# Optimization experiments

Measured on AMD Instinct MI355X. Metric: run time of the kernel, lower is better.

The kernel has to match this reference:

```python
import jax, jax.numpy as jnp
import numpy as np
import math

EMB, HID, SEQ, BATCH, VOCAB, LAYERS = 512, 1024, 128, 64, 10000, 2


def setup_inputs() -> dict:
    key = jax.random.key(0)
    ks = jax.random.split(key, 8)
    bnd = math.sqrt(1.0 / HID)
    return {
        "inputs": jax.random.randint(ks[0], (SEQ, BATCH), 0, VOCAB),
        "hidden": jnp.zeros((LAYERS, BATCH, HID), jnp.float32),
        "emb": jax.random.uniform(ks[1], (VOCAB, EMB), jnp.float32, -0.1, 0.1),
        "W_x0": jax.random.uniform(ks[2], (EMB, HID), jnp.float32, -bnd, bnd),
        "W_x1": jax.random.uniform(ks[3], (HID, HID), jnp.float32, -bnd, bnd),
        "W_h": jax.random.uniform(ks[4], (LAYERS, HID, HID), jnp.float32, -bnd, bnd),
        "b_h": jax.random.uniform(ks[5], (LAYERS, HID), jnp.float32, -bnd, bnd),
        "W_out": jax.random.uniform(ks[6], (HID, VOCAB), jnp.float32, -0.1, 0.1),
        "b_out": jnp.zeros((VOCAB,), jnp.float32),
    }


def reference(inputs, hidden, emb, W_x0, W_x1, W_h, b_h, W_out, b_out):
    # Stacked vanilla RNN over time; dropout is identity (dp_keep_prob=1.0).
    scale = jnp.asarray(math.sqrt(EMB), jnp.float32)  # WordEmbedding * sqrt(n_units)

    def step(h, tok):
        # h: (L, B, H); tok: (B,)
        x = emb[tok] * scale                                   # (B, E)
        h0 = jnp.tanh(x @ W_x0 + h[0] @ W_h[0] + b_h[0])       # (B, H)
        h1 = jnp.tanh(h0 @ W_x1 + h[1] @ W_h[1] + b_h[1])      # (B, H)
        logits_t = h1 @ W_out + b_out                          # (B, V)
        return jnp.stack([h0, h1]), logits_t

    final_hidden, logits = jax.lax.scan(step, hidden, inputs)
    return logits, final_hidden
```

## Files before the change

kernel.cpp:

```cpp
#include <hip/hip_runtime.h>
#include <math.h>


typedef unsigned short u16;
typedef unsigned long long u64;
typedef __bf16 bf16x8 __attribute__((ext_vector_type(8)));
typedef float  f32x4  __attribute__((ext_vector_type(4)));
typedef unsigned int u32x4 __attribute__((ext_vector_type(4)));
typedef u16 u16x8 __attribute__((ext_vector_type(8)));

#define SEQ_ 128
#define B_   64
#define E_   512
#define H_   1024
#define V_   10000
#define VP_  10112
#define ROWS_ (SEQ_*B_)
#define BH_  (B_*H_)
#define LOGITS_ 81920000
#define NWG_ 192
#define FPS_ (129*32)

__device__ __forceinline__ u16 f2bf(float f) {
  unsigned u = __builtin_bit_cast(unsigned, f);
  u += 0x7fffu + ((u >> 16) & 1u);
  return (u16)(u >> 16);
}
__device__ __forceinline__ float bf2f(u16 h) {
  unsigned u = ((unsigned)h) << 16;
  return __builtin_bit_cast(float, u);
}
__device__ __forceinline__ void st64(void* p, u64 v) {
  __hip_atomic_store((u64*)p, v, __ATOMIC_RELAXED, __HIP_MEMORY_SCOPE_AGENT);
}
__device__ __forceinline__ u64 pk64(float a, float b) {
  return (u64)__builtin_bit_cast(unsigned, a) |
         ((u64)__builtin_bit_cast(unsigned, b) << 32);
}
__device__ __forceinline__ float tanh_fast(float x) {
  float e = __expf(2.0f * x);
  return 1.0f - 2.0f * __builtin_amdgcn_rcpf(e + 1.0f);
}


__global__ __launch_bounds__(256)
void transpose_split(const float* __restrict__ in, u16* __restrict__ outHi,
                     u16* __restrict__ outLo, int K, int N, int NP)
{
  __shared__ float tile[32][33];
  const int n0 = blockIdx.x * 32, k0 = blockIdx.y * 32;
  const int x = threadIdx.x & 31;
  const int y = threadIdx.x >> 5;
  (void)NP;
#pragma unroll
  for (int i = 0; i < 4; ++i) {
    const int r = y * 4 + i;
    const int n = n0 + x;
    tile[r][x] = (n < N) ? in[(size_t)(k0 + r) * N + n] : 0.f;
  }
  __syncthreads();
#pragma unroll
  for (int i = 0; i < 4; ++i) {
    const int r = y * 4 + i;
    const int n = n0 + r;
    const int k = k0 + x;
    const float v = tile[x][r];
    const u16 hb = f2bf(v);
    outHi[(size_t)n * K + k] = hb;
    if (outLo) outLo[(size_t)n * K + k] = f2bf(v - bf2f(hb));
  }
}

__global__ __launch_bounds__(256)
void gather_x(const int* __restrict__ toks, const float* __restrict__ emb,
              u16* __restrict__ XBhi, u16* __restrict__ XBlo)
{
  const int tid = blockIdx.x * 256 + threadIdx.x;
  const int row = tid >> 6;
  const int c8 = (tid & 63) * 8;
  const int tok = toks[row];
  const float* e = emb + (size_t)tok * E_ + c8;
  u16x8 hv, lv;
#pragma unroll
  for (int j = 0; j < 8; ++j) {
    float f = e[j] * 22.627416997969522f;
    u16 hb = f2bf(f);
    hv[j] = hb;
    lv[j] = f2bf(f - bf2f(hb));
  }
  *(u16x8*)(XBhi + (size_t)row * E_ + c8) = hv;
  *(u16x8*)(XBlo + (size_t)row * E_ + c8) = lv;
}

__global__ __launch_bounds__(256)
void hid_cast(const float* __restrict__ h, u16* H0hi, u16* H0lo, u16* H1hi, u16* H1lo)
{
  const int tid = blockIdx.x * 256 + threadIdx.x;
  float v0 = h[tid], v1 = h[BH_ + tid];
  u16 a = f2bf(v0); H0hi[tid] = a; H0lo[tid] = f2bf(v0 - bf2f(a));
  u16 b = f2bf(v1); H1hi[tid] = b; H1lo[tid] = f2bf(v1 - bf2f(b));
}

template<int NPASS>
__global__ __launch_bounds__(256)
void gemm_bf16(const u16* __restrict__ Ahi, const u16* __restrict__ Alo,
               const u16* __restrict__ Bhi, const u16* __restrict__ Blo,
               const float* __restrict__ bias, float* __restrict__ C,
               int K, int Nreal, int ldc, int nbx, int nby)
{
  constexpr int LDT = 40;
  __shared__ u16 lds[(NPASS == 3 ? 4 : 2) * 128 * LDT];
  u16* As  = lds;
  u16* Bs  = lds + 128 * LDT;
  u16* As2 = (NPASS == 3) ? (lds + 2 * 128 * LDT) : lds;
  u16* Bs2 = (NPASS == 3) ? (lds + 3 * 128 * LDT) : lds;

  const int S = 8;
  int bid  = blockIdx.x;
  int scol = bid / (S * nby);
  int rem  = bid - scol * (S * nby);
  int w    = nbx - scol * S; if (w > S) w = S;
  int bx   = scol * S + rem % w;
  int by   = rem / w;
  const int m0 = by * 128, n0 = bx * 128;

  const int tid  = threadIdx.x;
  const int wave = tid >> 6, lane = tid & 63;
  const int wm = (wave & 1) * 64, wn = (wave >> 1) * 64;
  const int lrow = lane & 15, lk = (lane >> 4) * 8;

  f32x4 acc[4][4] = {};

  const int kTiles = K >> 5;
  for (int kt = 0; kt < kTiles; ++kt) {
    const int k0 = kt << 5;
    __syncthreads();
#pragma unroll
    for (int c = tid; c < 512; c += 256) {
      const int row = c >> 2, kq = c & 3;
      const int l = row * LDT + kq * 8;
      *(u32x4*)(As + l) = *(const u32x4*)(Ahi + (size_t)(m0 + row) * K + k0 + kq * 8);
      *(u32x4*)(Bs + l) = *(const u32x4*)(Bhi + (size_t)(n0 + row) * K + k0 + kq * 8);
      if constexpr (NPASS == 3) {
        *(u32x4*)(As2 + l) = *(const u32x4*)(Alo + (size_t)(m0 + row) * K + k0 + kq * 8);
        *(u32x4*)(Bs2 + l) = *(const u32x4*)(Blo + (size_t)(n0 + row) * K + k0 + kq * 8);
      }
    }
    __syncthreads();
    bf16x8 a[4], b[4];
#pragma unroll
    for (int i = 0; i < 4; ++i) {
      a[i] = *(const bf16x8*)(As + (wm + i * 16 + lrow) * LDT + lk);
      b[i] = *(const bf16x8*)(Bs + (wn + i * 16 + lrow) * LDT + lk);
    }
    if constexpr (NPASS == 3) {
      bf16x8 a2[4], b2[4];
#pragma unroll
      for (int i = 0; i < 4; ++i) {
        a2[i] = *(const bf16x8*)(As2 + (wm + i * 16 + lrow) * LDT + lk);
        b2[i] = *(const bf16x8*)(Bs2 + (wn + i * 16 + lrow) * LDT + lk);
      }
#pragma unroll
      for (int mi = 0; mi < 4; ++mi)
#pragma unroll
        for (int ni = 0; ni < 4; ++ni) {
          acc[mi][ni] = __builtin_amdgcn_mfma_f32_16x16x32_bf16(a[mi],  b[ni],  acc[mi][ni], 0, 0, 0);
          acc[mi][ni] = __builtin_amdgcn_mfma_f32_16x16x32_bf16(a[mi],  b2[ni], acc[mi][ni], 0, 0, 0);
          acc[mi][ni] = __builtin_amdgcn_mfma_f32_16x16x32_bf16(a2[mi], b[ni],  acc[mi][ni], 0, 0, 0);
        }
    } else {
#pragma unroll
      for (int mi = 0; mi < 4; ++mi)
#pragma unroll
        for (int ni = 0; ni < 4; ++ni)
          acc[mi][ni] = __builtin_amdgcn_mfma_f32_16x16x32_bf16(a[mi], b[ni], acc[mi][ni], 0, 0, 0);
    }
  }
#pragma unroll
  for (int mi = 0; mi < 4; ++mi)
#pragma unroll
    for (int ni = 0; ni < 4; ++ni)
#pragma unroll
      for (int r = 0; r < 4; ++r) {
        const int row = m0 + wm + mi * 16 + (lane >> 4) * 4 + r;
        const int col = n0 + wn + ni * 16 + lrow;
        if (col < Nreal) {
          float v = acc[mi][ni][r];
          if (bias) v += bias[col];
          C[(size_t)row * ldc + col] = v;
        }
      }
}

__device__ __forceinline__ void publishWG(unsigned* f, int wgi)
{
  asm volatile("s_waitcnt vmcnt(0)" ::: "memory");
  __syncthreads();
  if (threadIdx.x == 0)
    __hip_atomic_store(f + wgi, 1u, __ATOMIC_RELAXED, __HIP_MEMORY_SCOPE_AGENT);
}
__device__ __forceinline__ void pollG(const unsigned* f)
{
  if (threadIdx.x < 64) {
    int it = 0;
    for (;;) {
      unsigned v = __hip_atomic_load(f + (threadIdx.x & 31),
                                     __ATOMIC_RELAXED, __HIP_MEMORY_SCOPE_AGENT);
      if (__all(v != 0)) break;
      if (it < 4) __builtin_amdgcn_s_sleep(2);
      else        __builtin_amdgcn_s_sleep(8);
      ++it;
    }
  }
  __syncthreads();
}
__device__ __forceinline__ void pollG2(const unsigned* fA, const unsigned* fB)
{
  if (threadIdx.x < 64) {
    int it = 0;
    bool okA = false, okB = false;
    for (;;) {
      const int l = threadIdx.x & 31;
      if (!okA) okA = __all(__hip_atomic_load(fA + l, __ATOMIC_RELAXED,
                                              __HIP_MEMORY_SCOPE_AGENT) != 0);
      if (!okB) okB = __all(__hip_atomic_load(fB + l, __ATOMIC_RELAXED,
                                              __HIP_MEMORY_SCOPE_AGENT) != 0);
      if (okA && okB) break;
      if (it < 4) __builtin_amdgcn_s_sleep(2);
      else        __builtin_amdgcn_s_sleep(8);
      ++it;
    }
  }
  __syncthreads();
}

__device__ __forceinline__ f32x4 gemm96(const u16* __restrict__ Ahi,
                                        const u16* __restrict__ Alo,
                                        const u16* bsp, int xorv, int lk8,
                                        size_t aoff, f32x4 acc0)
{
  f32x4 acc1 = {0.f, 0.f, 0.f, 0.f};
  f32x4 acc2 = {0.f, 0.f, 0.f, 0.f};
#pragma unroll
  for (int kc = 0; kc < 32; ++kc) {
    bf16x8 ah = *(const bf16x8*)(Ahi + aoff + kc * 32);
    bf16x8 al = *(const bf16x8*)(Alo + aoff + kc * 32);
    bf16x8 bh = *(const bf16x8*)(bsp + ((kc * 32 + lk8) ^ xorv));
    bf16x8 bl = *(const bf16x8*)(bsp + 32768 + ((kc * 32 + lk8) ^ xorv));
    acc0 = __builtin_amdgcn_mfma_f32_16x16x32_bf16(bh, ah, acc0, 0, 0, 0);
    acc1 = __builtin_amdgcn_mfma_f32_16x16x32_bf16(bl, ah, acc1, 0, 0, 0);
    acc2 = __builtin_amdgcn_mfma_f32_16x16x32_bf16(bh, al, acc2, 0, 0, 0);
  }
  return acc0 + acc1 + acc2;
}

__global__ __launch_bounds__(256, 1)
void recur_roles(const u16* __restrict__ Wh0h, const u16* __restrict__ Wh0l,
                 const u16* __restrict__ Wx1h, const u16* __restrict__ Wx1l,
                 const u16* __restrict__ Wh1h, const u16* __restrict__ Wh1l,
                 const float* __restrict__ XP0, const float* __restrict__ b1,
                 float* __restrict__ Pbuf,
                 u16* __restrict__ H0hi, u16* __restrict__ H0lo,
                 u16* __restrict__ H1hi, u16* __restrict__ H1lo,
                 float* __restrict__ final0, float* __restrict__ final1,
                 unsigned* __restrict__ flags)
{
  __shared__ u16 bsm[2 * 32 * 1024];

  const int wg   = blockIdx.x;
  const int role = wg >> 6;
  const int idx  = wg & 63;
  const int bg   = idx >> 5, cg = idx & 31;

  const u16* Bhi = (role == 0) ? Wh0h : (role == 1) ? Wx1h : Wh1h;
  const u16* Blo = (role == 0) ? Wh0l : (role == 1) ? Wx1l : Wh1l;

  const int tid  = threadIdx.x;
  const int wv   = tid >> 6, lane = tid & 63;
  const int wbg  = wv >> 1, wcg = wv & 1;
  const int lb   = lane & 15;
  const int lk8  = (lane >> 4) * 8;

  for (int c = tid; c < 8192; c += 256) {
    const int p   = c >> 12;
    const int cc  = c & 4095;
    const int col = cc >> 7;
    const int k8  = (cc & 127) * 8;
    u32x4 v = *(const u32x4*)((p ? Blo : Bhi) + (size_t)(cg * 32 + col) * H_ + k8);
    *(u32x4*)(bsm + p * 32768 + col * 1024 + (k8 ^ ((col & 7) << 3))) = v;
  }
  __syncthreads();

  const int batch = bg * 32 + wbg * 16 + lb;
  const int c0    = cg * 32 + wcg * 16 + (lk8 >> 1);
  const int colL  = wcg * 16 + lb;
  const int xorv  = (colL & 7) << 3;
  const u16* bsp  = bsm + colL * 1024;
  const size_t aoff = (size_t)batch * H_ + lk8;
  const size_t boff = (size_t)batch * H_ + c0;

  unsigned* flg0 = flags;
  unsigned* flgP = flags + 2 * FPS_;
  unsigned* flg1 = flags + 4 * FPS_;

  if (role == 0) {
    for (int t = 0; t < SEQ_; ++t) {
      f32x4 init = *(const f32x4*)(XP0 + (size_t)t * BH_ + boff);
      if (t >= 1) pollG(flg0 + ((size_t)bg * 129 + t) * 32);
      f32x4 acc = gemm96(H0hi + (size_t)t * BH_, H0lo + (size_t)t * BH_,
                         bsp, xorv, lk8, aoff, init);
      u64 whi = 0, wlo = 0; float hv[4];
#pragma unroll
      for (int r = 0; r < 4; ++r) {
        float v = tanh_fast(acc[r]);
        u16 hb = f2bf(v);
        whi |= (u64)hb << (16 * r);
        wlo |= (u64)f2bf(v - bf2f(hb)) << (16 * r);
        hv[r] = v;
      }
      st64(H0hi + (size_t)(t + 1) * BH_ + boff, whi);
      st64(H0lo + (size_t)(t + 1) * BH_ + boff, wlo);
      if (t == SEQ_ - 1) {
        st64(final0 + boff,     pk64(hv[0], hv[1]));
        st64(final0 + boff + 2, pk64(hv[2], hv[3]));
      }
      publishWG(flg0 + ((size_t)bg * 129 + (t + 1)) * 32, cg);
    }
  } else if (role == 1) {
    const f32x4 binit = *(const f32x4*)(b1 + c0);
    for (int s = 1; s <= SEQ_; ++s) {
      pollG(flg0 + ((size_t)bg * 129 + s) * 32);
      f32x4 acc = gemm96(H0hi + (size_t)s * BH_, H0lo + (size_t)s * BH_,
                         bsp, xorv, lk8, aoff, binit);
      float* op = Pbuf + (size_t)(s - 1) * BH_ + boff;
      st64(op,     pk64(acc[0], acc[1]));
      st64(op + 2, pk64(acc[2], acc[3]));
      publishWG(flgP + ((size_t)bg * 129 + s) * 32, cg);
    }
  } else {
    for (int s = 1; s <= SEQ_; ++s) {
      if (s >= 2) pollG2(flgP + ((size_t)bg * 129 + s) * 32,
                         flg1 + ((size_t)bg * 129 + (s - 1)) * 32);
      else        pollG (flgP + ((size_t)bg * 129 + s) * 32);
      f32x4 init = *(const f32x4*)(Pbuf + (size_t)(s - 1) * BH_ + boff);
      f32x4 acc = gemm96(H1hi + (size_t)(s - 1) * BH_, H1lo + (size_t)(s - 1) * BH_,
                         bsp, xorv, lk8, aoff, init);
      u64 whi = 0, wlo = 0; float hv[4];
#pragma unroll
      for (int r = 0; r < 4; ++r) {
        float v = tanh_fast(acc[r]);
        u16 hb = f2bf(v);
        whi |= (u64)hb << (16 * r);
        wlo |= (u64)f2bf(v - bf2f(hb)) << (16 * r);
        hv[r] = v;
      }
      st64(H1hi + (size_t)s * BH_ + boff, whi);
      st64(H1lo + (size_t)s * BH_ + boff, wlo);
      if (s == SEQ_) {
        st64(final1 + boff,     pk64(hv[0], hv[1]));
        st64(final1 + boff + 2, pk64(hv[2], hv[3]));
      }
      publishWG(flg1 + ((size_t)bg * 129 + s) * 32, cg);
    }
  }
}

extern "C" void kernel_launch(void* const* d_in, const int* in_sizes, int n_in,
                              void* d_out, int out_size, void* d_ws, size_t ws_size,
                              hipStream_t stream)
{
  (void)in_sizes; (void)n_in; (void)out_size; (void)ws_size;
  const int*   toks = (const int*)d_in[0];
  const float* hid0 = (const float*)d_in[1];
  const float* emb  = (const float*)d_in[2];
  const float* Wx0  = (const float*)d_in[3];
  const float* Wx1  = (const float*)d_in[4];
  const float* Wh   = (const float*)d_in[5];
  const float* bh   = (const float*)d_in[6];
  const float* Wout = (const float*)d_in[7];
  const float* bout = (const float*)d_in[8];
  float* out = (float*)d_out;

  char* ws = (char*)d_ws;
  size_t off = 0;
  auto alloc = [&](size_t bytes) -> void* {
    void* p = ws + off;
    off += (bytes + 255) & ~(size_t)255;
    return p;
  };
  unsigned* flags = (unsigned*)alloc(6 * FPS_ * 4);
  u16* XBhi  = (u16*)alloc((size_t)ROWS_ * E_ * 2);
  u16* XBlo  = (u16*)alloc((size_t)ROWS_ * E_ * 2);
  u16* Wx0Th = (u16*)alloc((size_t)H_ * E_ * 2);
  u16* Wx0Tl = (u16*)alloc((size_t)H_ * E_ * 2);
  u16* Wx1Th = (u16*)alloc((size_t)H_ * H_ * 2);
  u16* Wx1Tl = (u16*)alloc((size_t)H_ * H_ * 2);
  u16* Wh0Th = (u16*)alloc((size_t)H_ * H_ * 2);
  u16* Wh0Tl = (u16*)alloc((size_t)H_ * H_ * 2);
  u16* Wh1Th = (u16*)alloc((size_t)H_ * H_ * 2);
  u16* Wh1Tl = (u16*)alloc((size_t)H_ * H_ * 2);
  u16* WoutT = (u16*)alloc((size_t)VP_ * H_ * 2);
  float* XP0 = (float*)alloc((size_t)ROWS_ * H_ * 4);
  float* Pbuf= (float*)alloc((size_t)SEQ_ * BH_ * 4);
  u16* H0hi  = (u16*)alloc((size_t)(SEQ_ + 1) * BH_ * 2);
  u16* H0lo  = (u16*)alloc((size_t)(SEQ_ + 1) * BH_ * 2);
  u16* H1hi  = (u16*)alloc((size_t)(SEQ_ + 1) * BH_ * 2);
  u16* H1lo  = (u16*)alloc((size_t)(SEQ_ + 1) * BH_ * 2);

  hipMemsetAsync(flags, 0, 6 * FPS_ * 4, stream);
  transpose_split<<<dim3(H_ / 32, E_ / 32), 256, 0, stream>>>(Wx0, Wx0Th, Wx0Tl, E_, H_, H_);
  transpose_split<<<dim3(H_ / 32, H_ / 32), 256, 0, stream>>>(Wx1, Wx1Th, Wx1Tl, H_, H_, H_);
  transpose_split<<<dim3(H_ / 32, H_ / 32), 256, 0, stream>>>(Wh,           Wh0Th, Wh0Tl, H_, H_, H_);
  transpose_split<<<dim3(H_ / 32, H_ / 32), 256, 0, stream>>>(Wh + H_ * H_, Wh1Th, Wh1Tl, H_, H_, H_);
  transpose_split<<<dim3(VP_ / 32, H_ / 32), 256, 0, stream>>>(Wout, WoutT, nullptr, H_, V_, VP_);
  gather_x<<<ROWS_ * E_ / 8 / 256, 256, 0, stream>>>(toks, emb, XBhi, XBlo);
  hid_cast<<<BH_ / 256, 256, 0, stream>>>(hid0, H0hi, H0lo, H1hi, H1lo);

  gemm_bf16<3><<<8 * 64, 256, 0, stream>>>(XBhi, XBlo, Wx0Th, Wx0Tl, bh, XP0,
                                           E_, H_, H_, 8, 64);
  recur_roles<<<NWG_, 256, 0, stream>>>(Wh0Th, Wh0Tl, Wx1Th, Wx1Tl, Wh1Th, Wh1Tl,
                                        XP0, bh + H_, Pbuf,
                                        H0hi, H0lo, H1hi, H1lo,
                                        out + LOGITS_, out + LOGITS_ + BH_, flags);
  gemm_bf16<1><<<79 * 64, 256, 0, stream>>>(H1hi + BH_, nullptr, WoutT, nullptr,
                                            bout, out, H_, V_, V_, 79, 64);
}
```

Before: 2.027 ms.

## Map recurrence role groups to XCDs and poll same-XCD flags via L2

Launches 256 workgroups and uses the round-robin block-to-XCD assignment so each (role, batch-group) of 32 workgroups sits on one XCD, with two XCDs' worth of blocks exiting immediately. Flags produced and consumed within the same XCD are polled with sc0 loads that hit the shared L2, with a periodic agent-scope load as a fallback; cross-XCD waits keep agent-scope polling with shorter sleeps. The intent is lower step-to-step handoff latency in the serial recurrence. It relies on the undocumented dispatch order of blocks to XCDs and on L2 coherence for correctness and speed, and the H data written by other workgroups is still read through normal loads.

```diff
diff --git a/kernel.cpp b/kernel.cpp
--- a/kernel.cpp
+++ b/kernel.cpp
@@ -18,7 +18,6 @@
 #define ROWS_ (SEQ_*B_)
 #define BH_  (B_*H_)
 #define LOGITS_ 81920000
-#define NWG_ 192
 #define FPS_ (129*32)
 
 __device__ __forceinline__ u16 f2bf(float f) {
@@ -40,6 +39,13 @@
 __device__ __forceinline__ float tanh_fast(float x) {
   float e = __expf(2.0f * x);
   return 1.0f - 2.0f * __builtin_amdgcn_rcpf(e + 1.0f);
+}
+__device__ __forceinline__ unsigned ld_sc0(const unsigned* p) {
+  unsigned v;
+  asm volatile("global_load_dword %0, %1, off sc0\n\t"
+               "s_waitcnt vmcnt(0)"
+               : "=v"(v) : "v"(p) : "memory");
+  return v;
 }
 
 
@@ -199,35 +205,33 @@
   if (threadIdx.x == 0)
     __hip_atomic_store(f + wgi, 1u, __ATOMIC_RELAXED, __HIP_MEMORY_SCOPE_AGENT);
 }
-__device__ __forceinline__ void pollG(const unsigned* f)
+__device__ __forceinline__ void pollL(const unsigned* f)
 {
   if (threadIdx.x < 64) {
+    const int l = threadIdx.x & 31;
+    for (int it = 0;; ++it) {
+      unsigned v;
+      if ((it & 15) == 15)
+        v = __hip_atomic_load(f + l, __ATOMIC_RELAXED, __HIP_MEMORY_SCOPE_AGENT);
+      else
+        v = ld_sc0(f + l);
+      if (__all(v != 0)) break;
+      __builtin_amdgcn_s_sleep(1);
+    }
+  }
+  __syncthreads();
+}
+__device__ __forceinline__ void pollR(const unsigned* f)
+{
+  if (threadIdx.x < 64) {
+    const int l = threadIdx.x & 31;
     int it = 0;
     for (;;) {
-      unsigned v = __hip_atomic_load(f + (threadIdx.x & 31),
-                                     __ATOMIC_RELAXED, __HIP_MEMORY_SCOPE_AGENT);
+      unsigned v = __hip_atomic_load(f + l, __ATOMIC_RELAXED,
+                                     __HIP_MEMORY_SCOPE_AGENT);
       if (__all(v != 0)) break;
-      if (it < 4) __builtin_amdgcn_s_sleep(2);
-      else        __builtin_amdgcn_s_sleep(8);
-      ++it;
-    }
-  }
-  __syncthreads();
-}
-__device__ __forceinline__ void pollG2(const unsigned* fA, const unsigned* fB)
-{
-  if (threadIdx.x < 64) {
-    int it = 0;
-    bool okA = false, okB = false;
-    for (;;) {
-      const int l = threadIdx.x & 31;
-      if (!okA) okA = __all(__hip_atomic_load(fA + l, __ATOMIC_RELAXED,
-                                              __HIP_MEMORY_SCOPE_AGENT) != 0);
-      if (!okB) okB = __all(__hip_atomic_load(fB + l, __ATOMIC_RELAXED,
-                                              __HIP_MEMORY_SCOPE_AGENT) != 0);
-      if (okA && okB) break;
-      if (it < 4) __builtin_amdgcn_s_sleep(2);
-      else        __builtin_amdgcn_s_sleep(8);
+      if (it < 4) __builtin_amdgcn_s_sleep(1);
+      else        __builtin_amdgcn_s_sleep(4);
       ++it;
     }
   }
@@ -267,10 +271,12 @@
 {
   __shared__ u16 bsm[2 * 32 * 1024];
 
-  const int wg   = blockIdx.x;
-  const int role = wg >> 6;
-  const int idx  = wg & 63;
-  const int bg   = idx >> 5, cg = idx & 31;
+  const int bid  = blockIdx.x;
+  const int xcd  = bid & 7;
+  if (xcd >= 6) return;
+  const int role = xcd >> 1;
+  const int bg   = xcd & 1;
+  const int cg   = bid >> 3;
 
   const u16* Bhi = (role == 0) ? Wh0h : (role == 1) ? Wx1h : Wh1h;
   const u16* Blo = (role == 0) ? Wh0l : (role == 1) ? Wx1l : Wh1l;
@@ -306,7 +312,7 @@
   if (role == 0) {
     for (int t = 0; t < SEQ_; ++t) {
       f32x4 init = *(const f32x4*)(XP0 + (size_t)t * BH_ + boff);
-      if (t >= 1) pollG(flg0 + ((size_t)bg * 129 + t) * 32);
+      if (t >= 1) pollL(flg0 + ((size_t)bg * 129 + t) * 32);
       f32x4 acc = gemm96(H0hi + (size_t)t * BH_, H0lo + (size_t)t * BH_,
                          bsp, xorv, lk8, aoff, init);
       u64 whi = 0, wlo = 0; float hv[4];
@@ -329,7 +335,7 @@
   } else if (role == 1) {
     const f32x4 binit = *(const f32x4*)(b1 + c0);
     for (int s = 1; s <= SEQ_; ++s) {
-      pollG(flg0 + ((size_t)bg * 129 + s) * 32);
+      pollR(flg0 + ((size_t)bg * 129 + s) * 32);
       f32x4 acc = gemm96(H0hi + (size_t)s * BH_, H0lo + (size_t)s * BH_,
                          bsp, xorv, lk8, aoff, binit);
       float* op = Pbuf + (size_t)(s - 1) * BH_ + boff;
@@ -339,9 +345,8 @@
     }
   } else {
     for (int s = 1; s <= SEQ_; ++s) {
-      if (s >= 2) pollG2(flgP + ((size_t)bg * 129 + s) * 32,
-                         flg1 + ((size_t)bg * 129 + (s - 1)) * 32);
-      else        pollG (flgP + ((size_t)bg * 129 + s) * 32);
+      pollR(flgP + ((size_t)bg * 129 + s) * 32);
+      if (s >= 2) pollL(flg1 + ((size_t)bg * 129 + (s - 1)) * 32);
       f32x4 init = *(const f32x4*)(Pbuf + (size_t)(s - 1) * BH_ + boff);
       f32x4 acc = gemm96(H1hi + (size_t)(s - 1) * BH_, H1lo + (size_t)(s - 1) * BH_,
                          bsp, xorv, lk8, aoff, init);
@@ -418,10 +423,10 @@
 
   gemm_bf16<3><<<8 * 64, 256, 0, stream>>>(XBhi, XBlo, Wx0Th, Wx0Tl, bh, XP0,
                                            E_, H_, H_, 8, 64);
-  recur_roles<<<NWG_, 256, 0, stream>>>(Wh0Th, Wh0Tl, Wx1Th, Wx1Tl, Wh1Th, Wh1Tl,
-                                        XP0, bh + H_, Pbuf,
-                                        H0hi, H0lo, H1hi, H1lo,
-                                        out + LOGITS_, out + LOGITS_ + BH_, flags);
+  recur_roles<<<256, 256, 0, stream>>>(Wh0Th, Wh0Tl, Wx1Th, Wx1Tl, Wh1Th, Wh1Tl,
+                                       XP0, bh + H_, Pbuf,
+                                       H0hi, H0lo, H1hi, H1lo,
+                                       out + LOGITS_, out + LOGITS_ + BH_, flags);
   gemm_bf16<1><<<79 * 64, 256, 0, stream>>>(H1hi + BH_, nullptr, WoutT, nullptr,
                                             bout, out, H_, V_, V_, 79, 64);
 }
```

New measurement: 1.890 ms. -6.8%, faster.

## Fuse input projection, recurrence and output GEMM into one persistent megakernel

Applied to the files above, without the earlier changes.

Replaces the separate weight-transpose kernels, the input-projection GEMM, the role-based recurrence kernel and the final logits GEMM with one 256-workgroup persistent kernel. 192 workgroups run the layer recurrences in a wavefront schedule synchronised by a global counter barrier each step. The other 64 workgroups first stream the layer-0 input projection, publishing a per-timestep watermark, then compute logits for each timestep once its layer-1 hidden state is ready. The goal is to hide the input-projection and output GEMMs behind the serial recurrence and to cut launch and transpose overhead. In exchange, every recurrence step now waits on a full 192-workgroup barrier instead of per-batch-group flags. The logits GEMM also runs on only 64 workgroups with less tile reuse, so it may become the new critical path.

```diff
diff --git a/kernel.cpp b/kernel.cpp
--- a/kernel.cpp
+++ b/kernel.cpp
@@ -3,10 +3,11 @@
 
 
 typedef unsigned short u16;
+typedef unsigned int u32;
 typedef unsigned long long u64;
 typedef __bf16 bf16x8 __attribute__((ext_vector_type(8)));
 typedef float  f32x4  __attribute__((ext_vector_type(4)));
-typedef unsigned int u32x4 __attribute__((ext_vector_type(4)));
+typedef u32 u32x4 __attribute__((ext_vector_type(4)));
 typedef u16 u16x8 __attribute__((ext_vector_type(8)));
 
 #define SEQ_ 128
@@ -18,8 +19,6 @@
 #define ROWS_ (SEQ_*B_)
 #define BH_  (B_*H_)
 #define LOGITS_ 81920000
-#define NWG_ 192
-#define FPS_ (129*32)
 
 __device__ __forceinline__ u16 f2bf(float f) {
   unsigned u = __builtin_bit_cast(unsigned, f);
@@ -44,14 +43,13 @@
 
 
 __global__ __launch_bounds__(256)
-void transpose_split(const float* __restrict__ in, u16* __restrict__ outHi,
-                     u16* __restrict__ outLo, int K, int N, int NP)
+void transpose_bf16(const float* __restrict__ in, u16* __restrict__ outHi,
+                    int K, int N)
 {
   __shared__ float tile[32][33];
   const int n0 = blockIdx.x * 32, k0 = blockIdx.y * 32;
   const int x = threadIdx.x & 31;
   const int y = threadIdx.x >> 5;
-  (void)NP;
 #pragma unroll
   for (int i = 0; i < 4; ++i) {
     const int r = y * 4 + i;
@@ -62,12 +60,7 @@
 #pragma unroll
   for (int i = 0; i < 4; ++i) {
     const int r = y * 4 + i;
-    const int n = n0 + r;
-    const int k = k0 + x;
-    const float v = tile[x][r];
-    const u16 hb = f2bf(v);
-    outHi[(size_t)n * K + k] = hb;
-    if (outLo) outLo[(size_t)n * K + k] = f2bf(v - bf2f(hb));
+    outHi[(size_t)(n0 + r) * K + k0 + x] = f2bf(tile[x][r]);
   }
 }
 
@@ -101,134 +94,37 @@
   u16 b = f2bf(v1); H1hi[tid] = b; H1lo[tid] = f2bf(v1 - bf2f(b));
 }
 
-template<int NPASS>
-__global__ __launch_bounds__(256)
-void gemm_bf16(const u16* __restrict__ Ahi, const u16* __restrict__ Alo,
-               const u16* __restrict__ Bhi, const u16* __restrict__ Blo,
-               const float* __restrict__ bias, float* __restrict__ C,
-               int K, int Nreal, int ldc, int nbx, int nby)
-{
-  constexpr int LDT = 40;
-  __shared__ u16 lds[(NPASS == 3 ? 4 : 2) * 128 * LDT];
-  u16* As  = lds;
-  u16* Bs  = lds + 128 * LDT;
-  u16* As2 = (NPASS == 3) ? (lds + 2 * 128 * LDT) : lds;
-  u16* Bs2 = (NPASS == 3) ? (lds + 3 * 128 * LDT) : lds;
-
-  const int S = 8;
-  int bid  = blockIdx.x;
-  int scol = bid / (S * nby);
-  int rem  = bid - scol * (S * nby);
-  int w    = nbx - scol * S; if (w > S) w = S;
-  int bx   = scol * S + rem % w;
-  int by   = rem / w;
-  const int m0 = by * 128, n0 = bx * 128;
-
-  const int tid  = threadIdx.x;
-  const int wave = tid >> 6, lane = tid & 63;
-  const int wm = (wave & 1) * 64, wn = (wave >> 1) * 64;
-  const int lrow = lane & 15, lk = (lane >> 4) * 8;
-
-  f32x4 acc[4][4] = {};
-
-  const int kTiles = K >> 5;
-  for (int kt = 0; kt < kTiles; ++kt) {
-    const int k0 = kt << 5;
-    __syncthreads();
-#pragma unroll
-    for (int c = tid; c < 512; c += 256) {
-      const int row = c >> 2, kq = c & 3;
-      const int l = row * LDT + kq * 8;
-      *(u32x4*)(As + l) = *(const u32x4*)(Ahi + (size_t)(m0 + row) * K + k0 + kq * 8);
-      *(u32x4*)(Bs + l) = *(const u32x4*)(Bhi + (size_t)(n0 + row) * K + k0 + kq * 8);
-      if constexpr (NPASS == 3) {
-        *(u32x4*)(As2 + l) = *(const u32x4*)(Alo + (size_t)(m0 + row) * K + k0 + kq * 8);
-        *(u32x4*)(Bs2 + l) = *(const u32x4*)(Blo + (size_t)(n0 + row) * K + k0 + kq * 8);
-      }
-    }
-    __syncthreads();
-    bf16x8 a[4], b[4];
-#pragma unroll
-    for (int i = 0; i < 4; ++i) {
-      a[i] = *(const bf16x8*)(As + (wm + i * 16 + lrow) * LDT + lk);
-      b[i] = *(const bf16x8*)(Bs + (wn + i * 16 + lrow) * LDT + lk);
-    }
-    if constexpr (NPASS == 3) {
-      bf16x8 a2[4], b2[4];
-#pragma unroll
-      for (int i = 0; i < 4; ++i) {
-        a2[i] = *(const bf16x8*)(As2 + (wm + i * 16 + lrow) * LDT + lk);
-        b2[i] = *(const bf16x8*)(Bs2 + (wn + i * 16 + lrow) * LDT + lk);
-      }
-#pragma unroll
-      for (int mi = 0; mi < 4; ++mi)
-#pragma unroll
-        for (int ni = 0; ni < 4; ++ni) {
-          acc[mi][ni] = __builtin_amdgcn_mfma_f32_16x16x32_bf16(a[mi],  b[ni],  acc[mi][ni], 0, 0, 0);
-          acc[mi][ni] = __builtin_amdgcn_mfma_f32_16x16x32_bf16(a[mi],  b2[ni], acc[mi][ni], 0, 0, 0);
-          acc[mi][ni] = __builtin_amdgcn_mfma_f32_16x16x32_bf16(a2[mi], b[ni],  acc[mi][ni], 0, 0, 0);
-        }
-    } else {
-#pragma unroll
-      for (int mi = 0; mi < 4; ++mi)
-#pragma unroll
-        for (int ni = 0; ni < 4; ++ni)
-          acc[mi][ni] = __builtin_amdgcn_mfma_f32_16x16x32_bf16(a[mi], b[ni], acc[mi][ni], 0, 0, 0);
-    }
-  }
-#pragma unroll
-  for (int mi = 0; mi < 4; ++mi)
-#pragma unroll
-    for (int ni = 0; ni < 4; ++ni)
-#pragma unroll
-      for (int r = 0; r < 4; ++r) {
-        const int row = m0 + wm + mi * 16 + (lane >> 4) * 4 + r;
-        const int col = n0 + wn + ni * 16 + lrow;
-        if (col < Nreal) {
-          float v = acc[mi][ni][r];
-          if (bias) v += bias[col];
-          C[(size_t)row * ldc + col] = v;
-        }
-      }
-}
-
-__device__ __forceinline__ void publishWG(unsigned* f, int wgi)
+__device__ __forceinline__ void gbar(unsigned* flags, unsigned my)
 {
   asm volatile("s_waitcnt vmcnt(0)" ::: "memory");
   __syncthreads();
   if (threadIdx.x == 0)
-    __hip_atomic_store(f + wgi, 1u, __ATOMIC_RELAXED, __HIP_MEMORY_SCOPE_AGENT);
-}
-__device__ __forceinline__ void pollG(const unsigned* f)
-{
+    __hip_atomic_store(flags + blockIdx.x * 16u, my, __ATOMIC_RELAXED,
+                       __HIP_MEMORY_SCOPE_AGENT);
   if (threadIdx.x < 64) {
-    int it = 0;
+    const int l = threadIdx.x;
+    bool ok0 = false, ok1 = false, ok2 = false;
     for (;;) {
-      unsigned v = __hip_atomic_load(f + (threadIdx.x & 31),
-                                     __ATOMIC_RELAXED, __HIP_MEMORY_SCOPE_AGENT);
-      if (__all(v != 0)) break;
-      if (it < 4) __builtin_amdgcn_s_sleep(2);
-      else        __builtin_amdgcn_s_sleep(8);
-      ++it;
+      if (!ok0) ok0 = __hip_atomic_load(flags + l * 16,         __ATOMIC_RELAXED, __HIP_MEMORY_SCOPE_AGENT) >= my;
+      if (!ok1) ok1 = __hip_atomic_load(flags + (l + 64) * 16,  __ATOMIC_RELAXED, __HIP_MEMORY_SCOPE_AGENT) >= my;
+      if (!ok2) ok2 = __hip_atomic_load(flags + (l + 128) * 16, __ATOMIC_RELAXED, __HIP_MEMORY_SCOPE_AGENT) >= my;
+      if (__all(ok0 && ok1 && ok2)) break;
+      __builtin_amdgcn_s_sleep(2);
     }
   }
   __syncthreads();
 }
-__device__ __forceinline__ void pollG2(const unsigned* fA, const unsigned* fB)
+__device__ __forceinline__ void wait_flags(const unsigned* flags, unsigned tgt)
 {
   if (threadIdx.x < 64) {
-    int it = 0;
-    bool okA = false, okB = false;
+    const int l = threadIdx.x;
+    bool ok0 = false, ok1 = false, ok2 = false;
     for (;;) {
-      const int l = threadIdx.x & 31;
-      if (!okA) okA = __all(__hip_atomic_load(fA + l, __ATOMIC_RELAXED,
-                                              __HIP_MEMORY_SCOPE_AGENT) != 0);
-      if (!okB) okB = __all(__hip_atomic_load(fB + l, __ATOMIC_RELAXED,
-                                              __HIP_MEMORY_SCOPE_AGENT) != 0);
-      if (okA && okB) break;
-      if (it < 4) __builtin_amdgcn_s_sleep(2);
-      else        __builtin_amdgcn_s_sleep(8);
-      ++it;
+      if (!ok0) ok0 = __hip_atomic_load(flags + l * 16,         __ATOMIC_RELAXED, __HIP_MEMORY_SCOPE_AGENT) >= tgt;
+      if (!ok1) ok1 = __hip_atomic_load(flags + (l + 64) * 16,  __ATOMIC_RELAXED, __HIP_MEMORY_SCOPE_AGENT) >= tgt;
+      if (!ok2) ok2 = __hip_atomic_load(flags + (l + 128) * 16, __ATOMIC_RELAXED, __HIP_MEMORY_SCOPE_AGENT) >= tgt;
+      if (__all(ok0 && ok1 && ok2)) break;
+      __builtin_amdgcn_s_sleep(4);
     }
   }
   __syncthreads();
@@ -255,112 +151,212 @@
 }
 
 __global__ __launch_bounds__(256, 1)
-void recur_roles(const u16* __restrict__ Wh0h, const u16* __restrict__ Wh0l,
-                 const u16* __restrict__ Wx1h, const u16* __restrict__ Wx1l,
-                 const u16* __restrict__ Wh1h, const u16* __restrict__ Wh1l,
-                 const float* __restrict__ XP0, const float* __restrict__ b1,
-                 float* __restrict__ Pbuf,
-                 u16* __restrict__ H0hi, u16* __restrict__ H0lo,
-                 u16* __restrict__ H1hi, u16* __restrict__ H1lo,
-                 float* __restrict__ final0, float* __restrict__ final1,
-                 unsigned* __restrict__ flags)
+void rnn_mega(const float* __restrict__ Wh,
+              const float* __restrict__ Wx1f,
+              const float* __restrict__ Wx0f,
+              const u16*   __restrict__ WoutT,
+              const u16*   __restrict__ XBhi, const u16* __restrict__ XBlo,
+              const float* __restrict__ bh,
+              const float* __restrict__ bout,
+              float* __restrict__ XP0, float* __restrict__ Pbuf,
+              u16* __restrict__ H0hi, u16* __restrict__ H0lo,
+              u16* __restrict__ H1hi, u16* __restrict__ H1lo,
+              float* __restrict__ out,
+              float* __restrict__ final0, float* __restrict__ final1,
+              unsigned* __restrict__ flags, unsigned* __restrict__ xpcnt,
+              unsigned* __restrict__ xphw)
 {
   __shared__ u16 bsm[2 * 32 * 1024];
 
   const int wg   = blockIdx.x;
-  const int role = wg >> 6;
-  const int idx  = wg & 63;
-  const int bg   = idx >> 5, cg = idx & 31;
-
-  const u16* Bhi = (role == 0) ? Wh0h : (role == 1) ? Wx1h : Wh1h;
-  const u16* Blo = (role == 0) ? Wh0l : (role == 1) ? Wx1l : Wh1l;
-
   const int tid  = threadIdx.x;
   const int wv   = tid >> 6, lane = tid & 63;
-  const int wbg  = wv >> 1, wcg = wv & 1;
   const int lb   = lane & 15;
   const int lk8  = (lane >> 4) * 8;
 
-  for (int c = tid; c < 8192; c += 256) {
-    const int p   = c >> 12;
-    const int cc  = c & 4095;
-    const int col = cc >> 7;
-    const int k8  = (cc & 127) * 8;
-    u32x4 v = *(const u32x4*)((p ? Blo : Bhi) + (size_t)(cg * 32 + col) * H_ + k8);
-    *(u32x4*)(bsm + p * 32768 + col * 1024 + (k8 ^ ((col & 7) << 3))) = v;
-  }
-  __syncthreads();
-
-  const int batch = bg * 32 + wbg * 16 + lb;
-  const int c0    = cg * 32 + wcg * 16 + (lk8 >> 1);
-  const int colL  = wcg * 16 + lb;
-  const int xorv  = (colL & 7) << 3;
-  const u16* bsp  = bsm + colL * 1024;
-  const size_t aoff = (size_t)batch * H_ + lk8;
-  const size_t boff = (size_t)batch * H_ + c0;
-
-  unsigned* flg0 = flags;
-  unsigned* flgP = flags + 2 * FPS_;
-  unsigned* flg1 = flags + 4 * FPS_;
-
-  if (role == 0) {
-    for (int t = 0; t < SEQ_; ++t) {
-      f32x4 init = *(const f32x4*)(XP0 + (size_t)t * BH_ + boff);
-      if (t >= 1) pollG(flg0 + ((size_t)bg * 129 + t) * 32);
-      f32x4 acc = gemm96(H0hi + (size_t)t * BH_, H0lo + (size_t)t * BH_,
-                         bsp, xorv, lk8, aoff, init);
-      u64 whi = 0, wlo = 0; float hv[4];
-#pragma unroll
-      for (int r = 0; r < 4; ++r) {
-        float v = tanh_fast(acc[r]);
-        u16 hb = f2bf(v);
-        whi |= (u64)hb << (16 * r);
-        wlo |= (u64)f2bf(v - bf2f(hb)) << (16 * r);
-        hv[r] = v;
+  if (wg < 192) {
+    const int role = wg >> 6;
+    const int idx  = wg & 63;
+    const int bg   = idx >> 5, cg = idx & 31;
+
+    const float* Wsrc = (role == 0) ? Wh : (role == 1) ? Wx1f : (Wh + H_ * H_);
+    for (int j = tid; j < 32768; j += 256) {
+      const int k = j >> 5, c = j & 31;
+      const float v = Wsrc[(size_t)k * H_ + cg * 32 + c];
+      const u16 hb = f2bf(v);
+      const int ks = ((k & ~7) ^ ((c & 7) << 3)) | (k & 7);
+      bsm[c * 1024 + ks] = hb;
+      bsm[32768 + c * 1024 + ks] = f2bf(v - bf2f(hb));
+    }
+    __syncthreads();
+
+    const int wbg = wv >> 1, wcg = wv & 1;
+    const int batch = bg * 32 + wbg * 16 + lb;
+    const int c0    = cg * 32 + wcg * 16 + (lk8 >> 1);
+    const int colL  = wcg * 16 + lb;
+    const int xorv  = (colL & 7) << 3;
+    const u16* bsp  = bsm + colL * 1024;
+    const size_t aoff = (size_t)batch * H_ + lk8;
+    const size_t boff = (size_t)batch * H_ + c0;
+    const f32x4 binit = *(const f32x4*)(bh + H_ + c0);
+
+    unsigned xph = 0;
+    for (int i = 0; i < 130; ++i) {
+      if (role == 0) {
+        if (i < 128) {
+          const int t = i;
+          if (tid < 64) {
+            while (xph <= (unsigned)t) {
+              xph = __hip_atomic_load(xphw, __ATOMIC_RELAXED, __HIP_MEMORY_SCOPE_AGENT);
+              if (xph <= (unsigned)t) __builtin_amdgcn_s_sleep(2);
+            }
+          }
+          __syncthreads();
+          f32x4 init = *(const f32x4*)(XP0 + (size_t)t * BH_ + boff);
+          f32x4 acc = gemm96(H0hi + (size_t)t * BH_, H0lo + (size_t)t * BH_,
+                             bsp, xorv, lk8, aoff, init);
+          u64 whi = 0, wlo = 0; float hv[4];
+#pragma unroll
+          for (int r = 0; r < 4; ++r) {
+            float v = tanh_fast(acc[r]);
+            u16 hb = f2bf(v);
+            whi |= (u64)hb << (16 * r);
+            wlo |= (u64)f2bf(v - bf2f(hb)) << (16 * r);
+            hv[r] = v;
+          }
+          st64(H0hi + (size_t)(t + 1) * BH_ + boff, whi);
+          st64(H0lo + (size_t)(t + 1) * BH_ + boff, wlo);
+          if (t == SEQ_ - 1) {
+            st64(final0 + boff,     pk64(hv[0], hv[1]));
+            st64(final0 + boff + 2, pk64(hv[2], hv[3]));
+          }
+        }
+      } else if (role == 1) {
+        if (i >= 1 && i < 129) {
+          f32x4 acc = gemm96(H0hi + (size_t)i * BH_, H0lo + (size_t)i * BH_,
+                             bsp, xorv, lk8, aoff, binit);
+          float* op = Pbuf + (size_t)(i - 1) * BH_ + boff;
+          st64(op,     pk64(acc[0], acc[1]));
+          st64(op + 2, pk64(acc[2], acc[3]));
+        }
+      } else {
+        if (i >= 2) {
+          const int t = i - 2;
+          f32x4 init = *(const f32x4*)(Pbuf + (size_t)t * BH_ + boff);
+          f32x4 acc = gemm96(H1hi + (size_t)t * BH_, H1lo + (size_t)t * BH_,
+                             bsp, xorv, lk8, aoff, init);
+          u64 whi = 0, wlo = 0; float hv[4];
+#pragma unroll
+          for (int r = 0; r < 4; ++r) {
+            float v = tanh_fast(acc[r]);
+            u16 hb = f2bf(v);
+            whi |= (u64)hb << (16 * r);
+            wlo |= (u64)f2bf(v - bf2f(hb)) << (16 * r);
+            hv[r] = v;
+          }
+          st64(H1hi + (size_t)(t + 1) * BH_ + boff, whi);
+          st64(H1lo + (size_t)(t + 1) * BH_ + boff, wlo);
+          if (t == SEQ_ - 1) {
+            st64(final1 + boff,     pk64(hv[0], hv[1]));
+            st64(final1 + boff + 2, pk64(hv[2], hv[3]));
+          }
+        }
       }
-      st64(H0hi + (size_t)(t + 1) * BH_ + boff, whi);
-      st64(H0lo + (size_t)(t + 1) * BH_ + boff, wlo);
-      if (t == SEQ_ - 1) {
-        st64(final0 + boff,     pk64(hv[0], hv[1]));
-        st64(final0 + boff + 2, pk64(hv[2], hv[3]));
+      gbar(flags, (unsigned)(i + 1));
+    }
+  } else {
+    const int u = wg - 192;
+
+    for (int j = tid; j < 8192; j += 256) {
+      const int k = j >> 4, c = j & 15;
+      const float v = Wx0f[(size_t)k * H_ + u * 16 + c];
+      const u16 hb = f2bf(v);
+      const int ks = ((k & ~7) ^ ((c & 7) << 3)) | (k & 7);
+      bsm[c * 512 + ks] = hb;
+      bsm[8192 + c * 512 + ks] = f2bf(v - bf2f(hb));
+    }
+    __syncthreads();
+    {
+      const int xorv = (lb & 7) << 3;
+      const u16* bsp = bsm + lb * 512;
+      const f32x4 b0i = *(const f32x4*)(bh + u * 16 + (lk8 >> 1));
+      for (int t = 0; t < SEQ_; ++t) {
+        const int row = t * 64 + wv * 16 + lb;
+        const u16* Ah = XBhi + (size_t)row * E_ + lk8;
+        const u16* Al = XBlo + (size_t)row * E_ + lk8;
+        f32x4 a0 = b0i, a1 = {0,0,0,0}, a2 = {0,0,0,0};
+#pragma unroll
+        for (int kc = 0; kc < 16; ++kc) {
+          bf16x8 ah = *(const bf16x8*)(Ah + kc * 32);
+          bf16x8 al = *(const bf16x8*)(Al + kc * 32);
+          bf16x8 bhf = *(const bf16x8*)(bsp + ((kc * 32 + lk8) ^ xorv));
+          bf16x8 blf = *(const bf16x8*)(bsp + 8192 + ((kc * 32 + lk8) ^ xorv));
+          a0 = __builtin_amdgcn_mfma_f32_16x16x32_bf16(bhf, ah, a0, 0, 0, 0);
+          a1 = __builtin_amdgcn_mfma_f32_16x16x32_bf16(blf, ah, a1, 0, 0, 0);
+          a2 = __builtin_amdgcn_mfma_f32_16x16x32_bf16(bhf, al, a2, 0, 0, 0);
+        }
+        f32x4 acc = a0 + a1 + a2;
+        float* p = XP0 + (size_t)row * H_ + u * 16 + (lk8 >> 1);
+        st64(p,     pk64(acc[0], acc[1]));
+        st64(p + 2, pk64(acc[2], acc[3]));
+        asm volatile("s_waitcnt vmcnt(0)" ::: "memory");
+        __syncthreads();
+        if (tid == 0) {
+          unsigned old = __hip_atomic_fetch_add(xpcnt + t, 1u, __ATOMIC_RELAXED,
+                                                __HIP_MEMORY_SCOPE_AGENT);
+          if (old == 63u)
+            __hip_atomic_store(xphw, (unsigned)(t + 1), __ATOMIC_RELAXED,
+                               __HIP_MEMORY_SCOPE_AGENT);
+        }
       }
-      publishWG(flg0 + ((size_t)bg * 129 + (t + 1)) * 32, cg);
-    }
-  } else if (role == 1) {
-    const f32x4 binit = *(const f32x4*)(b1 + c0);
+    }
+
+    const int xorva = (lb & 7) << 3;
     for (int s = 1; s <= SEQ_; ++s) {
-      pollG(flg0 + ((size_t)bg * 129 + s) * 32);
-      f32x4 acc = gemm96(H0hi + (size_t)s * BH_, H0lo + (size_t)s * BH_,
-                         bsp, xorv, lk8, aoff, binit);
-      float* op = Pbuf + (size_t)(s - 1) * BH_ + boff;
-      st64(op,     pk64(acc[0], acc[1]));
-      st64(op + 2, pk64(acc[2], acc[3]));
-      publishWG(flgP + ((size_t)bg * 129 + s) * 32, cg);
-    }
-  } else {
-    for (int s = 1; s <= SEQ_; ++s) {
-      if (s >= 2) pollG2(flgP + ((size_t)bg * 129 + s) * 32,
-                         flg1 + ((size_t)bg * 129 + (s - 1)) * 32);
-      else        pollG (flgP + ((size_t)bg * 129 + s) * 32);
-      f32x4 init = *(const f32x4*)(Pbuf + (size_t)(s - 1) * BH_ + boff);
-      f32x4 acc = gemm96(H1hi + (size_t)(s - 1) * BH_, H1lo + (size_t)(s - 1) * BH_,
-                         bsp, xorv, lk8, aoff, init);
-      u64 whi = 0, wlo = 0; float hv[4];
-#pragma unroll
-      for (int r = 0; r < 4; ++r) {
-        float v = tanh_fast(acc[r]);
-        u16 hb = f2bf(v);
-        whi |= (u64)hb << (16 * r);
-        wlo |= (u64)f2bf(v - bf2f(hb)) << (16 * r);
-        hv[r] = v;
+      wait_flags(flags, (unsigned)(s + 2));
+      __syncthreads();
+      for (int c = tid; c < 8192; c += 256) {
+        const int row = c >> 7, ch = c & 127;
+        *(u16x8*)(bsm + row * 1024 + ((ch * 8) ^ ((row & 7) << 3))) =
+            *(const u16x8*)(H1hi + (size_t)s * BH_ + (size_t)row * H_ + ch * 8);
       }
-      st64(H1hi + (size_t)s * BH_ + boff, whi);
-      st64(H1lo + (size_t)s * BH_ + boff, wlo);
-      if (s == SEQ_) {
-        st64(final1 + boff,     pk64(hv[0], hv[1]));
-        st64(final1 + boff + 2, pk64(hv[2], hv[3]));
+      __syncthreads();
+#pragma unroll 1
+      for (int blk = 0; blk < 2; ++blk) {
+        const int nb = u + blk * 64;
+        if (nb >= 79) break;
+        f32x4 acc[4][2] = {};
+#pragma unroll
+        for (int kc = 0; kc < 32; ++kc) {
+          bf16x8 a[4], b[2];
+#pragma unroll
+          for (int mt = 0; mt < 4; ++mt)
+            a[mt] = *(const bf16x8*)(bsm + (mt * 16 + lb) * 1024 +
+                                     ((kc * 32 + lk8) ^ xorva));
+#pragma unroll
+          for (int nt = 0; nt < 2; ++nt)
+            b[nt] = *(const bf16x8*)(WoutT +
+                     (size_t)(nb * 128 + wv * 32 + nt * 16 + lb) * 1024 +
+                     kc * 32 + lk8);
+#pragma unroll
+          for (int mt = 0; mt < 4; ++mt)
+#pragma unroll
+            for (int nt = 0; nt < 2; ++nt)
+              acc[mt][nt] = __builtin_amdgcn_mfma_f32_16x16x32_bf16(
+                  a[mt], b[nt], acc[mt][nt], 0, 0, 0);
+        }
+#pragma unroll
+        for (int mt = 0; mt < 4; ++mt)
+#pragma unroll
+          for (int nt = 0; nt < 2; ++nt)
+#pragma unroll
+            for (int r = 0; r < 4; ++r) {
+              const int rowg = (s - 1) * 64 + mt * 16 + (lane >> 4) * 4 + r;
+              const int colg = nb * 128 + wv * 32 + nt * 16 + lb;
+              if (colg < V_)
+                out[(size_t)rowg * V_ + colg] = acc[mt][nt][r] + bout[colg];
+            }
       }
-      publishWG(flg1 + ((size_t)bg * 129 + s) * 32, cg);
     }
   }
 }
@@ -388,17 +384,11 @@
     off += (bytes + 255) & ~(size_t)255;
     return p;
   };
-  unsigned* flags = (unsigned*)alloc(6 * FPS_ * 4);
+  unsigned* flags = (unsigned*)alloc(192 * 16 * 4);
+  unsigned* xpcnt = (unsigned*)alloc(SEQ_ * 4 + 64);
+  unsigned* xphw  = xpcnt + SEQ_;
   u16* XBhi  = (u16*)alloc((size_t)ROWS_ * E_ * 2);
   u16* XBlo  = (u16*)alloc((size_t)ROWS_ * E_ * 2);
-  u16* Wx0Th = (u16*)alloc((size_t)H_ * E_ * 2);
-  u16* Wx0Tl = (u16*)alloc((size_t)H_ * E_ * 2);
-  u16* Wx1Th = (u16*)alloc((size_t)H_ * H_ * 2);
-  u16* Wx1Tl = (u16*)alloc((size_t)H_ * H_ * 2);
-  u16* Wh0Th = (u16*)alloc((size_t)H_ * H_ * 2);
-  u16* Wh0Tl = (u16*)alloc((size_t)H_ * H_ * 2);
-  u16* Wh1Th = (u16*)alloc((size_t)H_ * H_ * 2);
-  u16* Wh1Tl = (u16*)alloc((size_t)H_ * H_ * 2);
   u16* WoutT = (u16*)alloc((size_t)VP_ * H_ * 2);
   float* XP0 = (float*)alloc((size_t)ROWS_ * H_ * 4);
   float* Pbuf= (float*)alloc((size_t)SEQ_ * BH_ * 4);
@@ -407,21 +397,16 @@
   u16* H1hi  = (u16*)alloc((size_t)(SEQ_ + 1) * BH_ * 2);
   u16* H1lo  = (u16*)alloc((size_t)(SEQ_ + 1) * BH_ * 2);
 
-  hipMemsetAsync(flags, 0, 6 * FPS_ * 4, stream);
-  transpose_split<<<dim3(H_ / 32, E_ / 32), 256, 0, stream>>>(Wx0, Wx0Th, Wx0Tl, E_, H_, H_);
-  transpose_split<<<dim3(H_ / 32, H_ / 32), 256, 0, stream>>>(Wx1, Wx1Th, Wx1Tl, H_, H_, H_);
-  transpose_split<<<dim3(H_ / 32, H_ / 32), 256, 0, stream>>>(Wh,           Wh0Th, Wh0Tl, H_, H_, H_);
-  transpose_split<<<dim3(H_ / 32, H_ / 32), 256, 0, stream>>>(Wh + H_ * H_, Wh1Th, Wh1Tl, H_, H_, H_);
-  transpose_split<<<dim3(VP_ / 32, H_ / 32), 256, 0, stream>>>(Wout, WoutT, nullptr, H_, V_, VP_);
+  hipMemsetAsync(flags, 0, 192 * 16 * 4, stream);
+  hipMemsetAsync(xpcnt, 0, SEQ_ * 4 + 64, stream);
+
+  transpose_bf16<<<dim3(VP_ / 32, H_ / 32), 256, 0, stream>>>(Wout, WoutT, H_, V_);
   gather_x<<<ROWS_ * E_ / 8 / 256, 256, 0, stream>>>(toks, emb, XBhi, XBlo);
   hid_cast<<<BH_ / 256, 256, 0, stream>>>(hid0, H0hi, H0lo, H1hi, H1lo);
 
-  gemm_bf16<3><<<8 * 64, 256, 0, stream>>>(XBhi, XBlo, Wx0Th, Wx0Tl, bh, XP0,
-                                           E_, H_, H_, 8, 64);
-  recur_roles<<<NWG_, 256, 0, stream>>>(Wh0Th, Wh0Tl, Wx1Th, Wx1Tl, Wh1Th, Wh1Tl,
-                                        XP0, bh + H_, Pbuf,
-                                        H0hi, H0lo, H1hi, H1lo,
-                                        out + LOGITS_, out + LOGITS_ + BH_, flags);
-  gemm_bf16<1><<<79 * 64, 256, 0, stream>>>(H1hi + BH_, nullptr, WoutT, nullptr,
-                                            bout, out, H_, V_, V_, 79, 64);
-}
+  rnn_mega<<<256, 256, 0, stream>>>(Wh, Wx1, Wx0, WoutT, XBhi, XBlo,
+                                    bh, bout, XP0, Pbuf,
+                                    H0hi, H0lo, H1hi, H1lo,
+                                    out, out + LOGITS_, out + LOGITS_ + BH_,
+                                    flags, xpcnt, xphw);
+}
```

Measured after the change: 4.227 ms. 109% more time.
